# Kernel tuning notes

Measured on AMD Instinct MI355X. Metric: run time of the kernel, lower is better.

Reference implementation:

```python
import jax, jax.numpy as jnp
import numpy as np

B, N, D_IN, D_OUT, E = 4, 50000, 128, 128, 800000


def setup_inputs() -> dict:
    key = jax.random.key(0)
    k_x, k_w, k_b, k_r, k_c, k_v = jax.random.split(key, 6)
    stdv = 1.0 / np.sqrt(D_OUT)
    x = jax.random.normal(k_x, (B, N, D_IN), dtype=jnp.float32)
    weight = jax.random.uniform(k_w, (D_IN, D_OUT), jnp.float32, -stdv, stdv)
    bias = jax.random.uniform(k_b, (D_OUT,), jnp.float32, -stdv, stdv)
    adj_rows = jax.random.randint(k_r, (E,), 0, N, dtype=jnp.int32)
    adj_cols = jax.random.randint(k_c, (E,), 0, N, dtype=jnp.int32)
    # positive edge weights (e.g. normalized adjacency values)
    adj_vals = jax.random.uniform(k_v, (E,), jnp.float32) * (1.0 / 16.0)
    edge_index = jnp.stack([adj_rows, adj_cols]).astype(jnp.int64)  # unused (pyg_builtin=False)
    return {"input": x, "weight": weight, "bias": bias,
            "adj_vals": adj_vals, "adj_rows": adj_rows, "adj_cols": adj_cols,
            "edge_index": edge_index}


def reference(input, weight, bias, adj_vals, adj_rows, adj_cols, edge_index):
    # support = input @ W : [B, N, D_OUT]
    support = jnp.einsum('bnd,df->bnf', input, weight)

    # node_repr = sparse adj (COO) @ support, batched == torch.sparse.mm path
    def agg(s):  # s: [N, D_OUT]
        msgs = adj_vals[:, None] * s[adj_cols]          # [E, D_OUT] gather
        return jax.ops.segment_sum(msgs, adj_rows, num_segments=N)  # scatter-add

    node_repr = jax.vmap(agg)(support) + bias           # [B, N, D_OUT]
    # net_norm='none' -> no norm; activation=relu; residual=False; dropout=0
    return jax.nn.relu(node_repr)
```

## Files before the change

kernel.cpp:

```cpp
#include <hip/hip_runtime.h>
#include <hip/hip_bf16.h>

#define BB 4
#define NN 50000
#define DIN 128
#define DOUT 128
#define EE 800000
#define TOTROWS (BB * NN)
#define LDA 136

#define NGB ((TOTROWS + 127) / 128)
#define NHB ((EE + 255) / 256)
#define CHUNK 1024
#define NCHUNK ((NN + CHUNK - 1) / CHUNK)
#define NPB 64
#define PAD8(x) (((x) + 7) & ~7)
#define EPK_CAP (EE + 8 * NN)

typedef unsigned short u16;
typedef unsigned int u32;

using shortx8 = __attribute__((ext_vector_type(8))) short;
using ushortx4 = __attribute__((ext_vector_type(4))) unsigned short;
using ushortx8 = __attribute__((ext_vector_type(8))) unsigned short;
using floatx4 = __attribute__((ext_vector_type(4))) float;

__device__ __forceinline__ float b2f(u16 u) {
    u32 x = ((u32)u) << 16;
    float f;
    __builtin_memcpy(&f, &x, 4);
    return f;
}

__device__ __forceinline__ u16 f2b(float f) {
    u32 x;
    __builtin_memcpy(&x, &f, 4);
    u32 r = x + 0x7fffu + ((x >> 16) & 1u);
    return (u16)(r >> 16);
}

__global__ __launch_bounds__(256)
void k1_detect_hist(const u16* __restrict__ X, const u16* __restrict__ W,
                    const u16* __restrict__ Bs, const u16* __restrict__ V,
                    int nx, int nw, int nb, int nv, int* __restrict__ flags,
                    const int* __restrict__ rows, int* __restrict__ deg) {
    if (blockIdx.x == 0) {
        __shared__ int cnt[4];
        const int t = threadIdx.x;
        const int w = t >> 6;
        const int l = t & 63;
        if (t < 4) cnt[t] = 0;
        __syncthreads();
        const u16* p = (w == 0) ? X : (w == 1) ? W : (w == 2) ? Bs : V;
        const int n  = (w == 0) ? nx : (w == 1) ? nw : (w == 2) ? nb : nv;
        int bad = 0;
        for (int k = 0; k < 4; ++k) {
            unsigned idx = 2u * (unsigned)(((unsigned long long)(l * 4 + k) *
                                            (unsigned)(n >> 1)) >> 8);
            u16 s = p[idx];
            unsigned e = (s >> 7) & 0xFF;
            bool ok = ((s & 0x7FFF) == 0) || (e >= 90 && e <= 141);
            bad += ok ? 0 : 1;
        }
        atomicAdd(&cnt[w], bad);
        __syncthreads();
        if (l == 0) flags[w] = (cnt[w] >= 77) ? 1 : 0;
    } else {
        int e = (int)(blockIdx.x - 1) * 256 + threadIdx.x;
        if (e < EE) atomicAdd(&deg[rows[e]], 1);
    }
}

__global__ __launch_bounds__(256)
void k2_scanred_prep(const int* __restrict__ deg, int* __restrict__ bsum,
                     const void* __restrict__ Wv, const int* __restrict__ flags,
                     u16* __restrict__ Wt) {
    if (blockIdx.x < NCHUNK) {
        __shared__ int sh[256];
        int t = threadIdx.x, blk = blockIdx.x;
        int base = blk * CHUNK + t * 4;
        int s = 0;
#pragma unroll
        for (int i = 0; i < 4; ++i) {
            int idx = base + i;
            if (idx < NN) s += PAD8(deg[idx]);
        }
        sh[t] = s;
        __syncthreads();
        for (int d = 128; d > 0; d >>= 1) {
            if (t < d) sh[t] += sh[t + d];
            __syncthreads();
        }
        if (t == 0) bsum[blk] = sh[0];
    } else {
        int t = (int)(blockIdx.x - NCHUNK) * 256 + threadIdx.x;
        if (t < DIN * DOUT) {
            int f = t >> 7, k = t & 127;
            size_t src = (size_t)k * DOUT + f;
            Wt[t] = flags[1] ? f2b(((const float*)Wv)[src]) : ((const u16*)Wv)[src];
        }
    }
}

__global__ __launch_bounds__(64)
void k_scan_base(const int* __restrict__ bsum, int* __restrict__ bbase,
                 int* __restrict__ off) {
    int l = threadIdx.x;
    int orig = (l < NCHUNK) ? bsum[l] : 0;
    int v = orig;
    for (int d = 1; d < 64; d <<= 1) {
        int x = __shfl_up(v, d);
        if (l >= d) v += x;
    }
    if (l < NCHUNK) bbase[l] = v - orig;
    if (l == NCHUNK - 1) off[NN] = v;
}

__global__ __launch_bounds__(256)
void k_scan_chunk(const int* __restrict__ deg, const int* __restrict__ bbase,
                  int* __restrict__ off) {
    __shared__ int sh[256];
    int t = threadIdx.x;
    int blk = blockIdx.x;
    int base = blk * CHUNK + t * 4;
    int v[4];
    int tsum = 0;
#pragma unroll
    for (int i = 0; i < 4; ++i) {
        int idx = base + i;
        v[i] = (idx < NN) ? PAD8(deg[idx]) : 0;
        tsum += v[i];
    }
    sh[t] = tsum;
    __syncthreads();
    for (int d = 1; d < 256; d <<= 1) {
        int x = (t >= d) ? sh[t - d] : 0;
        __syncthreads();
        sh[t] += x;
        __syncthreads();
    }
    int run = sh[t] - tsum + bbase[blk];
#pragma unroll
    for (int i = 0; i < 4; ++i) {
        int idx = base + i;
        if (idx < NN) off[idx] = run;
        run += v[i];
    }
}

__global__ __launch_bounds__(256, 3)
void k5_gemm_scatter(const void* __restrict__ Xv, const u16* __restrict__ Wt,
                     const int* __restrict__ flags, u16* __restrict__ sup,
                     const int* __restrict__ rows, const int* __restrict__ cols,
                     const void* __restrict__ valsv, const int* __restrict__ off,
                     int* __restrict__ cur, int2* __restrict__ epk) {
    if (blockIdx.x >= NGB) {
        int e = (int)(blockIdx.x - NGB) * 256 + threadIdx.x;
        if (e < EE) {
            int vf32 = flags[3];
            float v = vf32 ? ((const float*)valsv)[e]
                           : b2f(((const u16*)valsv)[e]);
            int r = rows[e];
            int p = off[r] + atomicAdd(&cur[r], 1);
            epk[p] = make_int2(cols[e], __float_as_int(v));
        }
        return;
    }

    __shared__ u16 lA[128 * LDA];

    const int xf32 = flags[0];
    const int tid = threadIdx.x;
    const int wid = tid >> 6;
    const int l   = tid & 63;
    const long rowBase = (long)blockIdx.x * 128;

    if (xf32) {
        const float* Xf = (const float*)Xv;
#pragma unroll
        for (int i = 0; i < 16; ++i) {
            int elem = i * 1024 + tid * 4;
            int row = elem >> 7, col = elem & 127;
            long gRow = rowBase + row;
            ushortx4 w4 = (ushortx4){0, 0, 0, 0};
            if (gRow < TOTROWS) {
                float4 v = *(const float4*)(Xf + gRow * DIN + col);
                w4[0] = f2b(v.x); w4[1] = f2b(v.y);
                w4[2] = f2b(v.z); w4[3] = f2b(v.w);
            }
            *(ushortx4*)&lA[row * LDA + col] = w4;
        }
    } else {
        const u16* X16 = (const u16*)Xv;
#pragma unroll
        for (int i = 0; i < 8; ++i) {
            int elem = i * 2048 + tid * 8;
            int row = elem >> 7, col = elem & 127;
            long gRow = rowBase + row;
            ushortx8 w8 = (ushortx8){0, 0, 0, 0, 0, 0, 0, 0};
            if (gRow < TOTROWS)
                w8 = *(const ushortx8*)(X16 + gRow * DIN + col);
            *(ushortx8*)&lA[row * LDA + col] = w8;
        }
    }

    const int wx = wid & 1;
    const int wy = wid >> 1;
    const int q8 = (l >> 4) * 8;
    const int lm = l & 15;

    shortx8 bf[16];
#pragma unroll
    for (int nt = 0; nt < 4; ++nt) {
        const size_t Frow = (size_t)(wx * 64 + nt * 16 + lm) * DIN;
#pragma unroll
        for (int c = 0; c < 4; ++c)
            bf[nt * 4 + c] = *(const shortx8*)(Wt + Frow + 32 * c + q8);
    }

    floatx4 acc[4][4];
#pragma unroll
    for (int mt = 0; mt < 4; ++mt)
#pragma unroll
        for (int nt = 0; nt < 4; ++nt)
            acc[mt][nt] = (floatx4){0.f, 0.f, 0.f, 0.f};

    __syncthreads();

    for (int c = 0; c < 4; ++c) {
        shortx8 af[4];
#pragma unroll
        for (int mt = 0; mt < 4; ++mt)
            af[mt] = *(const shortx8*)
                &lA[(size_t)(wy * 64 + mt * 16 + lm) * LDA + 32 * c + q8];
#pragma unroll
        for (int mt = 0; mt < 4; ++mt)
#pragma unroll
            for (int nt = 0; nt < 4; ++nt)
                acc[mt][nt] = __builtin_amdgcn_mfma_f32_16x16x32_bf16(
                    af[mt], bf[nt * 4 + c], acc[mt][nt], 0, 0, 0);
    }

    __syncthreads();
#pragma unroll
    for (int mt = 0; mt < 4; ++mt) {
#pragma unroll
        for (int reg = 0; reg < 4; ++reg) {
            int row = wy * 64 + mt * 16 + (l >> 4) * 4 + reg;
#pragma unroll
            for (int nt = 0; nt < 4; ++nt)
                lA[row * LDA + wx * 64 + nt * 16 + lm] = f2b(acc[mt][nt][reg]);
        }
    }
    __syncthreads();

#pragma unroll
    for (int i = 0; i < 8; ++i) {
        int elem = i * 2048 + tid * 8;
        int row = elem >> 7, col = elem & 127;
        long R = rowBase + row;
        if (R < TOTROWS) {
            int b = (int)(R / NN);
            int n = (int)(R % NN);
            ushortx8 v = *(const ushortx8*)&lA[row * LDA + col];
            *(ushortx8*)(sup + ((size_t)n * BB + b) * DOUT + col) = v;
        }
    }
}

__global__ __launch_bounds__(256)
void k_agg(const u16* __restrict__ sup, const int* __restrict__ off,
           const int2* __restrict__ epk, const void* __restrict__ biasv,
           const int* __restrict__ flags, float* __restrict__ out) {
    const int wid = threadIdx.x >> 6;
    const int l   = threadIdx.x & 63;
    const int n = blockIdx.x * 4 + wid;
    if (n >= NN) return;

    const int p0 = __builtin_amdgcn_readfirstlane(off[n]);
    const int p1 = __builtin_amdgcn_readfirstlane(off[n + 1]);

    float acc[8] = {0.f, 0.f, 0.f, 0.f, 0.f, 0.f, 0.f, 0.f};
    const int b  = l >> 4;
    const int f0 = (l & 15) * 8;
    const int lofs = l * 8;

    for (int pb = p0; pb < p1; pb += 64) {
        const int cnt = min(64, p1 - pb);
        int2 d = make_int2(0, 0);
        if (l < cnt) d = epk[pb + l];
        for (int j = 0; j < cnt; j += 8) {
            int   cs[8];
            float vs[8];
#pragma unroll
            for (int q = 0; q < 8; ++q) {
                cs[q] = __builtin_amdgcn_readlane(d.x, j + q);
                vs[q] = __int_as_float(__builtin_amdgcn_readlane(d.y, j + q));
            }
            ushortx8 sv[8];
#pragma unroll
            for (int q = 0; q < 8; ++q)
                sv[q] = *(const ushortx8*)(sup + (size_t)cs[q] * 512 + lofs);
#pragma unroll
            for (int q = 0; q < 8; ++q)
#pragma unroll
                for (int t = 0; t < 8; ++t)
                    acc[t] += vs[q] * b2f(sv[q][t]);
        }
    }

    float bb[8];
    if (flags[2]) {
        float4 bv1 = *(const float4*)((const float*)biasv + f0);
        float4 bv2 = *(const float4*)((const float*)biasv + f0 + 4);
        bb[0] = bv1.x; bb[1] = bv1.y; bb[2] = bv1.z; bb[3] = bv1.w;
        bb[4] = bv2.x; bb[5] = bv2.y; bb[6] = bv2.z; bb[7] = bv2.w;
    } else {
        ushortx8 bv = *(const ushortx8*)((const u16*)biasv + f0);
#pragma unroll
        for (int t = 0; t < 8; ++t) bb[t] = b2f(bv[t]);
    }

    float r[8];
#pragma unroll
    for (int t = 0; t < 8; ++t) r[t] = fmaxf(acc[t] + bb[t], 0.f);

    float* op = out + ((size_t)b * NN + n) * DOUT + f0;
    *(float4*)op       = (float4){r[0], r[1], r[2], r[3]};
    *(float4*)(op + 4) = (float4){r[4], r[5], r[6], r[7]};
}

extern "C" void kernel_launch(void* const* d_in, const int* in_sizes, int n_in,
                              void* d_out, int out_size, void* d_ws, size_t ws_size,
                              hipStream_t stream) {
    const void* X    = d_in[0];
    const void* W    = d_in[1];
    const void* bias = d_in[2];
    const void* vals = d_in[3];
    const int* rows  = (const int*)d_in[4];
    const int* cols  = (const int*)d_in[5];
    float* out = (float*)d_out;

    char* base = (char*)d_ws;
    size_t o = 0;
    int* flags = (int*)(base + o); o += 64;
    int* deg = (int*)(base + o); o += (size_t)NN * 4;
    int* cur = (int*)(base + o); o += (size_t)NN * 4;
    o = (o + 255) & ~(size_t)255;
    int* bsum  = (int*)(base + o); o += 64 * 4;
    int* bbase = (int*)(base + o); o += 64 * 4;
    o = (o + 255) & ~(size_t)255;
    u16* Wt = (u16*)(base + o); o += (size_t)DIN * DOUT * 2;
    o = (o + 255) & ~(size_t)255;
    int* off = (int*)(base + o); o += (size_t)(NN + 1) * 4;
    o = (o + 255) & ~(size_t)255;
    int2* epk = (int2*)(base + o); o += (size_t)EPK_CAP * 8;
    o = (o + 255) & ~(size_t)255;
    u16* sup = (u16*)(base + o); o += (size_t)BB * NN * DOUT * 2;
    (void)ws_size;

    hipMemsetAsync(deg, 0, (size_t)2 * NN * 4, stream);
    hipMemsetAsync(epk, 0, (size_t)EPK_CAP * 8, stream);

    k1_detect_hist<<<1 + NHB, 256, 0, stream>>>(
        (const u16*)X, (const u16*)W, (const u16*)bias, (const u16*)vals,
        in_sizes[0], in_sizes[1], in_sizes[2], in_sizes[3], flags, rows, deg);
    k2_scanred_prep<<<NCHUNK + NPB, 256, 0, stream>>>(deg, bsum, W, flags, Wt);
    k_scan_base<<<1, 64, 0, stream>>>(bsum, bbase, off);
    k_scan_chunk<<<NCHUNK, 256, 0, stream>>>(deg, bbase, off);
    k5_gemm_scatter<<<NGB + NHB, 256, 0, stream>>>(
        X, Wt, flags, sup, rows, cols, vals, off, cur, epk);
    k_agg<<<(NN + 3) / 4, 256, 0, stream>>>(sup, off, epk, bias, flags, out);
}
```

Before: 405.9 us.

## Drop edge padding, merge scan into one block, sort edges per chunk in aggregation

Removes the 8-edge padding of CSR segments, so the large memset of the packed edge buffer goes away, and collapses the three-kernel prefix scan into a single-block scan fused with the weight-transpose kernel. The aggregation kernel now bitonic-sorts each 64-edge chunk by column index across lanes so that gathers are more ordered, and it processes 16 edges per batch with sentinel padding. It also puts scatter blocks ahead of GEMM blocks in the combined launch and uses nontemporal stores for the support and output writes and a nontemporal load for the edge list. The cost is a serial single-block scan and extra shuffle work for the sort, plus wasted gathers of row 0 on padded slots.

```diff
diff --git a/kernel.cpp b/kernel.cpp
--- a/kernel.cpp
+++ b/kernel.cpp
@@ -11,11 +11,8 @@
 
 #define NGB ((TOTROWS + 127) / 128)
 #define NHB ((EE + 255) / 256)
-#define CHUNK 1024
-#define NCHUNK ((NN + CHUNK - 1) / CHUNK)
 #define NPB 64
-#define PAD8(x) (((x) + 7) & ~7)
-#define EPK_CAP (EE + 8 * NN)
+#define SCHUNK 196
 
 typedef unsigned short u16;
 typedef unsigned int u32;
@@ -72,28 +69,37 @@
 }
 
 __global__ __launch_bounds__(256)
-void k2_scanred_prep(const int* __restrict__ deg, int* __restrict__ bsum,
-                     const void* __restrict__ Wv, const int* __restrict__ flags,
-                     u16* __restrict__ Wt) {
-    if (blockIdx.x < NCHUNK) {
+void k2_scan_prep(const int* __restrict__ deg, int* __restrict__ off,
+                  const void* __restrict__ Wv, const int* __restrict__ flags,
+                  u16* __restrict__ Wt) {
+    if (blockIdx.x == 0) {
         __shared__ int sh[256];
-        int t = threadIdx.x, blk = blockIdx.x;
-        int base = blk * CHUNK + t * 4;
+        const int t = threadIdx.x;
+        const int c0 = t * SCHUNK;
         int s = 0;
-#pragma unroll
-        for (int i = 0; i < 4; ++i) {
-            int idx = base + i;
-            if (idx < NN) s += PAD8(deg[idx]);
+        for (int i = 0; i < SCHUNK; ++i) {
+            int idx = c0 + i;
+            if (idx < NN) s += deg[idx];
         }
         sh[t] = s;
         __syncthreads();
-        for (int d = 128; d > 0; d >>= 1) {
-            if (t < d) sh[t] += sh[t + d];
+        for (int d = 1; d < 256; d <<= 1) {
+            int x = (t >= d) ? sh[t - d] : 0;
             __syncthreads();
-        }
-        if (t == 0) bsum[blk] = sh[0];
+            sh[t] += x;
+            __syncthreads();
+        }
+        int run = (t > 0) ? sh[t - 1] : 0;
+        for (int i = 0; i < SCHUNK; ++i) {
+            int idx = c0 + i;
+            if (idx < NN) {
+                off[idx] = run;
+                run += deg[idx];
+            }
+        }
+        if (t == 255) off[NN] = sh[255];
     } else {
-        int t = (int)(blockIdx.x - NCHUNK) * 256 + threadIdx.x;
+        int t = (int)(blockIdx.x - 1) * 256 + threadIdx.x;
         if (t < DIN * DOUT) {
             int f = t >> 7, k = t & 127;
             size_t src = (size_t)k * DOUT + f;
@@ -102,60 +108,14 @@
     }
 }
 
-__global__ __launch_bounds__(64)
-void k_scan_base(const int* __restrict__ bsum, int* __restrict__ bbase,
-                 int* __restrict__ off) {
-    int l = threadIdx.x;
-    int orig = (l < NCHUNK) ? bsum[l] : 0;
-    int v = orig;
-    for (int d = 1; d < 64; d <<= 1) {
-        int x = __shfl_up(v, d);
-        if (l >= d) v += x;
-    }
-    if (l < NCHUNK) bbase[l] = v - orig;
-    if (l == NCHUNK - 1) off[NN] = v;
-}
-
-__global__ __launch_bounds__(256)
-void k_scan_chunk(const int* __restrict__ deg, const int* __restrict__ bbase,
-                  int* __restrict__ off) {
-    __shared__ int sh[256];
-    int t = threadIdx.x;
-    int blk = blockIdx.x;
-    int base = blk * CHUNK + t * 4;
-    int v[4];
-    int tsum = 0;
-#pragma unroll
-    for (int i = 0; i < 4; ++i) {
-        int idx = base + i;
-        v[i] = (idx < NN) ? PAD8(deg[idx]) : 0;
-        tsum += v[i];
-    }
-    sh[t] = tsum;
-    __syncthreads();
-    for (int d = 1; d < 256; d <<= 1) {
-        int x = (t >= d) ? sh[t - d] : 0;
-        __syncthreads();
-        sh[t] += x;
-        __syncthreads();
-    }
-    int run = sh[t] - tsum + bbase[blk];
-#pragma unroll
-    for (int i = 0; i < 4; ++i) {
-        int idx = base + i;
-        if (idx < NN) off[idx] = run;
-        run += v[i];
-    }
-}
-
 __global__ __launch_bounds__(256, 3)
-void k5_gemm_scatter(const void* __restrict__ Xv, const u16* __restrict__ Wt,
+void k5_scatter_gemm(const void* __restrict__ Xv, const u16* __restrict__ Wt,
                      const int* __restrict__ flags, u16* __restrict__ sup,
                      const int* __restrict__ rows, const int* __restrict__ cols,
                      const void* __restrict__ valsv, const int* __restrict__ off,
                      int* __restrict__ cur, int2* __restrict__ epk) {
-    if (blockIdx.x >= NGB) {
-        int e = (int)(blockIdx.x - NGB) * 256 + threadIdx.x;
+    if (blockIdx.x < NHB) {
+        int e = (int)blockIdx.x * 256 + threadIdx.x;
         if (e < EE) {
             int vf32 = flags[3];
             float v = vf32 ? ((const float*)valsv)[e]
@@ -173,7 +133,7 @@
     const int tid = threadIdx.x;
     const int wid = tid >> 6;
     const int l   = tid & 63;
-    const long rowBase = (long)blockIdx.x * 128;
+    const long rowBase = (long)(blockIdx.x - NHB) * 128;
 
     if (xf32) {
         const float* Xf = (const float*)Xv;
@@ -263,7 +223,8 @@
             int b = (int)(R / NN);
             int n = (int)(R % NN);
             ushortx8 v = *(const ushortx8*)&lA[row * LDA + col];
-            *(ushortx8*)(sup + ((size_t)n * BB + b) * DOUT + col) = v;
+            __builtin_nontemporal_store(
+                v, (ushortx8*)(sup + ((size_t)n * BB + b) * DOUT + col));
         }
     }
 }
@@ -287,22 +248,42 @@
 
     for (int pb = p0; pb < p1; pb += 64) {
         const int cnt = min(64, p1 - pb);
-        int2 d = make_int2(0, 0);
-        if (l < cnt) d = epk[pb + l];
-        for (int j = 0; j < cnt; j += 8) {
-            int   cs[8];
-            float vs[8];
-#pragma unroll
-            for (int q = 0; q < 8; ++q) {
-                cs[q] = __builtin_amdgcn_readlane(d.x, j + q);
-                vs[q] = __int_as_float(__builtin_amdgcn_readlane(d.y, j + q));
+        int x = 0x7FFFFFFF;
+        int y = 0;
+        if (l < cnt) {
+            long long d = __builtin_nontemporal_load(
+                (const long long*)(epk + pb + l));
+            x = (int)(d & 0xFFFFFFFFLL);
+            y = (int)(d >> 32);
+        }
+#pragma unroll
+        for (int k = 2; k <= 64; k <<= 1) {
+#pragma unroll
+            for (int j = k >> 1; j > 0; j >>= 1) {
+                int px = __shfl_xor(x, j);
+                int py = __shfl_xor(y, j);
+                bool keepMin = ((l & k) == 0) == ((l & j) == 0);
+                bool take = keepMin ? (px < x) : (px > x);
+                x = take ? px : x;
+                y = take ? py : y;
             }
-            ushortx8 sv[8];
-#pragma unroll
-            for (int q = 0; q < 8; ++q)
+        }
+        const int cnt16 = (cnt + 15) & ~15;
+        for (int j = 0; j < cnt16; j += 16) {
+            int   cs[16];
+            float vs[16];
+#pragma unroll
+            for (int q = 0; q < 16; ++q) {
+                int c = __builtin_amdgcn_readlane(x, j + q);
+                cs[q] = (c == 0x7FFFFFFF) ? 0 : c;
+                vs[q] = __int_as_float(__builtin_amdgcn_readlane(y, j + q));
+            }
+            ushortx8 sv[16];
+#pragma unroll
+            for (int q = 0; q < 16; ++q)
                 sv[q] = *(const ushortx8*)(sup + (size_t)cs[q] * 512 + lofs);
 #pragma unroll
-            for (int q = 0; q < 8; ++q)
+            for (int q = 0; q < 16; ++q)
 #pragma unroll
                 for (int t = 0; t < 8; ++t)
                     acc[t] += vs[q] * b2f(sv[q][t]);
@@ -321,13 +302,15 @@
         for (int t = 0; t < 8; ++t) bb[t] = b2f(bv[t]);
     }
 
-    float r[8];
-#pragma unroll
-    for (int t = 0; t < 8; ++t) r[t] = fmaxf(acc[t] + bb[t], 0.f);
+    floatx4 r0, r1;
+#pragma unroll
+    for (int t = 0; t < 4; ++t) r0[t] = fmaxf(acc[t] + bb[t], 0.f);
+#pragma unroll
+    for (int t = 0; t < 4; ++t) r1[t] = fmaxf(acc[t + 4] + bb[t + 4], 0.f);
 
     float* op = out + ((size_t)b * NN + n) * DOUT + f0;
-    *(float4*)op       = (float4){r[0], r[1], r[2], r[3]};
-    *(float4*)(op + 4) = (float4){r[4], r[5], r[6], r[7]};
+    __builtin_nontemporal_store(r0, (floatx4*)op);
+    __builtin_nontemporal_store(r1, (floatx4*)(op + 4));
 }
 
 extern "C" void kernel_launch(void* const* d_in, const int* in_sizes, int n_in,
@@ -347,28 +330,22 @@
     int* deg = (int*)(base + o); o += (size_t)NN * 4;
     int* cur = (int*)(base + o); o += (size_t)NN * 4;
     o = (o + 255) & ~(size_t)255;
-    int* bsum  = (int*)(base + o); o += 64 * 4;
-    int* bbase = (int*)(base + o); o += 64 * 4;
-    o = (o + 255) & ~(size_t)255;
     u16* Wt = (u16*)(base + o); o += (size_t)DIN * DOUT * 2;
     o = (o + 255) & ~(size_t)255;
     int* off = (int*)(base + o); o += (size_t)(NN + 1) * 4;
     o = (o + 255) & ~(size_t)255;
-    int2* epk = (int2*)(base + o); o += (size_t)EPK_CAP * 8;
+    int2* epk = (int2*)(base + o); o += (size_t)EE * 8;
     o = (o + 255) & ~(size_t)255;
     u16* sup = (u16*)(base + o); o += (size_t)BB * NN * DOUT * 2;
     (void)ws_size;
 
     hipMemsetAsync(deg, 0, (size_t)2 * NN * 4, stream);
-    hipMemsetAsync(epk, 0, (size_t)EPK_CAP * 8, stream);
 
     k1_detect_hist<<<1 + NHB, 256, 0, stream>>>(
         (const u16*)X, (const u16*)W, (const u16*)bias, (const u16*)vals,
         in_sizes[0], in_sizes[1], in_sizes[2], in_sizes[3], flags, rows, deg);
-    k2_scanred_prep<<<NCHUNK + NPB, 256, 0, stream>>>(deg, bsum, W, flags, Wt);
-    k_scan_base<<<1, 64, 0, stream>>>(bsum, bbase, off);
-    k_scan_chunk<<<NCHUNK, 256, 0, stream>>>(deg, bbase, off);
-    k5_gemm_scatter<<<NGB + NHB, 256, 0, stream>>>(
+    k2_scan_prep<<<1 + NPB, 256, 0, stream>>>(deg, off, W, flags, Wt);
+    k5_scatter_gemm<<<NHB + NGB, 256, 0, stream>>>(
         X, Wt, flags, sup, rows, cols, vals, off, cur, epk);
     k_agg<<<(NN + 3) / 4, 256, 0, stream>>>(sup, off, epk, bias, flags, out);
 }
```

After: 513.5 us. 1.27x slower.

## Split aggregation into two feature-half passes with nontemporal edge loads and stores

Applied to the files above, without the earlier changes.

The aggregation kernel now launches twice as many blocks, and each pass handles one 64-wide half of the output features. Each lane gathers 4 bf16 values (8 bytes) per edge instead of 8, so each node's edge list is read and traversed twice. This is meant to raise parallelism and shrink the per-pass gather footprint so the second pass may hit in cache. Edge-list loads and output stores become nontemporal to cut cache pollution, at the cost of redundant index reads and narrower memory transactions.

```diff
diff --git a/kernel.cpp b/kernel.cpp
--- a/kernel.cpp
+++ b/kernel.cpp
@@ -16,6 +16,7 @@
 #define NPB 64
 #define PAD8(x) (((x) + 7) & ~7)
 #define EPK_CAP (EE + 8 * NN)
+#define NAB (NN / 4)
 
 typedef unsigned short u16;
 typedef unsigned int u32;
@@ -272,23 +273,30 @@
 void k_agg(const u16* __restrict__ sup, const int* __restrict__ off,
            const int2* __restrict__ epk, const void* __restrict__ biasv,
            const int* __restrict__ flags, float* __restrict__ out) {
+    int blk = blockIdx.x;
+    const int pass = (blk >= NAB) ? 1 : 0;
+    if (pass) blk -= NAB;
     const int wid = threadIdx.x >> 6;
     const int l   = threadIdx.x & 63;
-    const int n = blockIdx.x * 4 + wid;
-    if (n >= NN) return;
+    const int n = blk * 4 + wid;
 
     const int p0 = __builtin_amdgcn_readfirstlane(off[n]);
     const int p1 = __builtin_amdgcn_readfirstlane(off[n + 1]);
 
-    float acc[8] = {0.f, 0.f, 0.f, 0.f, 0.f, 0.f, 0.f, 0.f};
+    float acc[4] = {0.f, 0.f, 0.f, 0.f};
     const int b  = l >> 4;
-    const int f0 = (l & 15) * 8;
-    const int lofs = l * 8;
+    const int f0 = pass * 64 + (l & 15) * 4;
+    const int lofs = b * 128 + f0;
 
     for (int pb = p0; pb < p1; pb += 64) {
         const int cnt = min(64, p1 - pb);
         int2 d = make_int2(0, 0);
-        if (l < cnt) d = epk[pb + l];
+        if (l < cnt) {
+            long long dv = __builtin_nontemporal_load(
+                (const long long*)(epk + pb + l));
+            d.x = (int)(dv & 0xFFFFFFFFLL);
+            d.y = (int)(dv >> 32);
+        }
         for (int j = 0; j < cnt; j += 8) {
             int   cs[8];
             float vs[8];
@@ -297,37 +305,34 @@
                 cs[q] = __builtin_amdgcn_readlane(d.x, j + q);
                 vs[q] = __int_as_float(__builtin_amdgcn_readlane(d.y, j + q));
             }
-            ushortx8 sv[8];
+            ushortx4 sv[8];
 #pragma unroll
             for (int q = 0; q < 8; ++q)
-                sv[q] = *(const ushortx8*)(sup + (size_t)cs[q] * 512 + lofs);
+                sv[q] = *(const ushortx4*)(sup + (size_t)cs[q] * 512 + lofs);
 #pragma unroll
             for (int q = 0; q < 8; ++q)
 #pragma unroll
-                for (int t = 0; t < 8; ++t)
+                for (int t = 0; t < 4; ++t)
                     acc[t] += vs[q] * b2f(sv[q][t]);
         }
     }
 
-    float bb[8];
+    float bb[4];
     if (flags[2]) {
-        float4 bv1 = *(const float4*)((const float*)biasv + f0);
-        float4 bv2 = *(const float4*)((const float*)biasv + f0 + 4);
-        bb[0] = bv1.x; bb[1] = bv1.y; bb[2] = bv1.z; bb[3] = bv1.w;
-        bb[4] = bv2.x; bb[5] = bv2.y; bb[6] = bv2.z; bb[7] = bv2.w;
+        float4 bv = *(const float4*)((const float*)biasv + f0);
+        bb[0] = bv.x; bb[1] = bv.y; bb[2] = bv.z; bb[3] = bv.w;
     } else {
-        ushortx8 bv = *(const ushortx8*)((const u16*)biasv + f0);
-#pragma unroll
-        for (int t = 0; t < 8; ++t) bb[t] = b2f(bv[t]);
-    }
-
-    float r[8];
-#pragma unroll
-    for (int t = 0; t < 8; ++t) r[t] = fmaxf(acc[t] + bb[t], 0.f);
+        ushortx4 bv = *(const ushortx4*)((const u16*)biasv + f0);
+#pragma unroll
+        for (int t = 0; t < 4; ++t) bb[t] = b2f(bv[t]);
+    }
+
+    floatx4 r;
+#pragma unroll
+    for (int t = 0; t < 4; ++t) r[t] = fmaxf(acc[t] + bb[t], 0.f);
 
     float* op = out + ((size_t)b * NN + n) * DOUT + f0;
-    *(float4*)op       = (float4){r[0], r[1], r[2], r[3]};
-    *(float4*)(op + 4) = (float4){r[4], r[5], r[6], r[7]};
+    __builtin_nontemporal_store(r, (floatx4*)op);
 }
 
 extern "C" void kernel_launch(void* const* d_in, const int* in_sizes, int n_in,
@@ -370,5 +375,5 @@
     k_scan_chunk<<<NCHUNK, 256, 0, stream>>>(deg, bbase, off);
     k5_gemm_scatter<<<NGB + NHB, 256, 0, stream>>>(
         X, Wt, flags, sup, rows, cols, vals, off, cur, epk);
-    k_agg<<<(NN + 3) / 4, 256, 0, stream>>>(sup, off, epk, bias, flags, out);
-}
+    k_agg<<<2 * NAB, 256, 0, stream>>>(sup, off, epk, bias, flags, out);
+}
```

Result: no change. 400.9 us (-1.2%).
